# Kernel optimization log

Hardware: AMD Instinct MI355X
Metric: run time of the kernel (lower is better)

The kernel has to match this reference:

```python
import jax, jax.numpy as jnp
import numpy as np
from jax import lax

T, B = 64, 16
N, W, R = 256, 64, 4          # mem_slot, mem_size, read_heads
IN, OUT = 64, 64
NHID, NNOUT = 256, 256
IF_SIZE = W * R + 3 * W + 5 * R + 3  # 471
EPS = 1e-6


def setup_inputs() -> dict:
    key = jax.random.key(0)
    ks = jax.random.split(key, 8)
    in_dim = IN + R * W
    def glorot(k, shape):
        fan_in = shape[0]
        return jax.random.normal(k, shape, dtype=jnp.float32) / np.sqrt(fan_in)
    return {
        "input_data": jax.random.normal(ks[0], (T, B, IN), dtype=jnp.float32),
        "W1": glorot(ks[1], (in_dim, NHID)),
        "b1": jnp.zeros((NHID,), jnp.float32),
        "W2": glorot(ks[2], (NHID, NNOUT)),
        "b2": jnp.zeros((NNOUT,), jnp.float32),
        "W_if": glorot(ks[3], (NNOUT, IF_SIZE)),
        "b_if": jnp.zeros((IF_SIZE,), jnp.float32),
        "W_out": glorot(ks[4], (NNOUT, OUT)),
        "W_mem_out": glorot(ks[5], (R * W, OUT)),
    }


def oneplus(x):
    return 1.0 + jax.nn.softplus(x)


def content_address(mem, keys, strengths):
    # mem [B,N,W], keys [B,W,R], strengths [B,R] -> weights [B,N,R]
    mem_n = mem / (jnp.linalg.norm(mem, axis=-1, keepdims=True) + EPS)
    key_n = keys / (jnp.linalg.norm(keys, axis=1, keepdims=True) + EPS)
    sim = jnp.einsum('bnw,bwr->bnr', mem_n, key_n)
    return jax.nn.softmax(sim * strengths[:, None, :], axis=1)


def parse_interface(z):
    # z: [B, IF_SIZE] -> dict of interface components (NeuCom layout)
    o = 0
    read_keys = z[:, o:o + W * R].reshape(-1, W, R); o += W * R
    read_str = oneplus(z[:, o:o + R]); o += R
    write_key = z[:, o:o + W]; o += W
    write_str = oneplus(z[:, o:o + 1]); o += 1
    erase = jax.nn.sigmoid(z[:, o:o + W]); o += W
    write_vec = z[:, o:o + W]; o += W
    free_gates = jax.nn.sigmoid(z[:, o:o + R]); o += R
    alloc_gate = jax.nn.sigmoid(z[:, o:o + 1]); o += 1
    write_gate = jax.nn.sigmoid(z[:, o:o + 1]); o += 1
    read_modes = jax.nn.softmax(z[:, o:o + 3 * R].reshape(-1, 3, R), axis=1)
    return (read_keys, read_str, write_key, write_str, erase, write_vec,
            free_gates, alloc_gate, write_gate, read_modes)


def _dnc_forward(input_data, W1, b1, W2, b2, W_if, b_if, W_out, W_mem_out):
    Bz = input_data.shape[1]
    eye = jnp.eye(N, dtype=input_data.dtype)

    def step(carry, x_t):
        mem, usage, rw, ww, prec, link, rvec = carry
        # --- controller (feedforward) ---
        ctrl_in = jnp.concatenate([x_t, rvec.reshape(Bz, R * W)], axis=1)
        h = jnp.tanh(ctrl_in @ W1 + b1)
        nn_out = jnp.tanh(h @ W2 + b2)
        (read_keys, read_str, write_key, write_str, erase, write_vec,
         free_gates, alloc_gate, write_gate, read_modes) = parse_interface(nn_out @ W_if + b_if)
        # --- write ---
        retention = jnp.prod(1.0 - free_gates[:, None, :] * rw, axis=2)   # [B,N]
        usage = (usage + ww - usage * ww) * retention
        idx = jnp.argsort(usage, axis=1)                                  # ascending usage
        u_sorted = jnp.take_along_axis(usage, idx, axis=1)
        prod_excl = jnp.concatenate(
            [jnp.ones((Bz, 1), usage.dtype), jnp.cumprod(u_sorted, axis=1)[:, :-1]], axis=1)
        alloc_sorted = (1.0 - u_sorted) * prod_excl
        alloc = jnp.take_along_axis(alloc_sorted, jnp.argsort(idx, axis=1), axis=1)
        wc = content_address(mem, write_key[:, :, None], write_str)[:, :, 0]  # [B,N]
        ww = write_gate * (alloc_gate * alloc + (1.0 - alloc_gate) * wc)
        mem = mem * (1.0 - ww[:, :, None] * erase[:, None, :]) \
              + ww[:, :, None] * write_vec[:, None, :]
        link = (1.0 - ww[:, :, None] - ww[:, None, :]) * link \
               + ww[:, :, None] * prec[:, None, :]
        link = link * (1.0 - eye)
        prec = (1.0 - jnp.sum(ww, axis=1, keepdims=True)) * prec + ww
        # --- read ---
        rc = content_address(mem, read_keys, read_str)                    # [B,N,R]
        fwd_w = jnp.einsum('bnm,bmr->bnr', link, rw)
        bwd_w = jnp.einsum('bmn,bmr->bnr', link, rw)
        rw = (bwd_w * read_modes[:, 0][:, None, :]
              + rc * read_modes[:, 1][:, None, :]
              + fwd_w * read_modes[:, 2][:, None, :])
        rvec = jnp.einsum('bnw,bnr->bwr', mem, rw)                        # [B,W,R]
        out = nn_out @ W_out + rvec.reshape(Bz, R * W) @ W_mem_out
        view = (free_gates, alloc_gate, write_gate, rw, ww, usage)
        return (mem, usage, rw, ww, prec, link, rvec), (out, view)

    carry0 = (
        jnp.full((Bz, N, W), EPS, input_data.dtype),   # mem_mat
        jnp.zeros((Bz, N), input_data.dtype),          # usage
        jnp.zeros((Bz, N, R), input_data.dtype),       # read_weight
        jnp.zeros((Bz, N), input_data.dtype),          # write_weight
        jnp.zeros((Bz, N), input_data.dtype),          # precedence
        jnp.zeros((Bz, N, N), input_data.dtype),       # link matrix
        jnp.zeros((Bz, W, R), input_data.dtype),       # read vectors
    )
    _, (outputs, _view) = lax.scan(step, carry0, input_data)
    return outputs  # [T,B,OUT]


def reference(input_data, W1, b1, W2, b2, W_if, b_if, W_out, W_mem_out):
    return _dnc_forward(input_data, W1, b1, W2, b2, W_if, b_if, W_out, W_mem_out)
```

## Files before the change

kernel.cpp:

```cpp
#include <hip/hip_runtime.h>
#include <hip/hip_fp16.h>
#include <math.h>

#define Tt 64
#define Bb 16
#define Nn 256
#define Ww 64
#define Rr 4
#define INd 64
#define OUTd 64
#define IFS 471
#define EPSf 1e-6f

#define W1OFF   0
#define W2OFF   40960
#define WIFOFF  73728
#define WOUTOFF 134016
#define WMEMOFF 142208
#define WTOT    150400

#define LROW    130
#define LINKB   (256 * LROW * 4)
#define SCRB    16384
#define FIXF    3456
#define SMEM_MAIN (LINKB + SCRB + FIXF * 4)
#define SMEM_FB   (SCRB + FIXF * 4)

#define RWS 132

typedef _Float16 h2v __attribute__((ext_vector_type(2)));
__device__ __forceinline__ float fdot2(__half2 a, __half2 b, float c) {
    return __builtin_amdgcn_fdot2(*(h2v*)&a, *(h2v*)&b, c, false);
}
__device__ __forceinline__ __half2 pkh(float a, float b) {
    auto r = __builtin_amdgcn_cvt_pkrtz(a, b);
    return *(__half2*)&r;
}

__device__ __forceinline__ float rcpf(float x) {
#if __has_builtin(__builtin_amdgcn_rcpf)
    return __builtin_amdgcn_rcpf(x);
#else
    return 1.f / x;
#endif
}
__device__ __forceinline__ float sigm(float x) { return rcpf(1.f + __expf(-x)); }
__device__ __forceinline__ float tanh_fast(float x) {
    float xc = fminf(fmaxf(x, -15.f), 15.f);
    float e = __expf(2.f * xc);
    return (e - 1.f) * rcpf(e + 1.f);
}
__device__ __forceinline__ float oneplus_(float x) {
    return 1.f + fmaxf(x, 0.f) + log1pf(expf(-fabsf(x)));
}
__device__ __forceinline__ float wsum(float v) {
#pragma unroll
    for (int o = 32; o; o >>= 1) v += __shfl_xor(v, o, 64);
    return v;
}
__device__ __forceinline__ float wmaxr(float v) {
#pragma unroll
    for (int o = 32; o; o >>= 1) v = fmaxf(v, __shfl_xor(v, o, 64));
    return v;
}

__device__ __attribute__((noinline)) float gemv_part(
    const __half2* __restrict__ wP, int str, int iters,
    const __half2* __restrict__ vin)
{
    float a[8] = {0.f,0.f,0.f,0.f,0.f,0.f,0.f,0.f};
    float4 h0 = *(const float4*)(wP);
    float4 h1 = *(const float4*)(wP + str);
#pragma unroll 1
    for (int j0 = 0; j0 < iters - 8; j0 += 8) {
        int k8n = (j0 >> 2) + 2;
        float4 n0 = *(const float4*)(wP + (size_t)k8n * str);
        float4 n1 = *(const float4*)(wP + (size_t)(k8n + 1) * str);
        float4 v0 = *(const float4*)(vin + j0);
        float4 v1 = *(const float4*)(vin + j0 + 4);
        const __half2* hh0 = (const __half2*)&h0;
        const __half2* hh1 = (const __half2*)&h1;
        const __half2* vv0 = (const __half2*)&v0;
        const __half2* vv1 = (const __half2*)&v1;
#pragma unroll
        for (int u = 0; u < 4; ++u) a[u]     = fdot2(hh0[u], vv0[u], a[u]);
#pragma unroll
        for (int u = 0; u < 4; ++u) a[4 + u] = fdot2(hh1[u], vv1[u], a[4 + u]);
        h0 = n0; h1 = n1;
    }
    {
        float4 v0 = *(const float4*)(vin + iters - 8);
        float4 v1 = *(const float4*)(vin + iters - 4);
        const __half2* hh0 = (const __half2*)&h0;
        const __half2* hh1 = (const __half2*)&h1;
        const __half2* vv0 = (const __half2*)&v0;
        const __half2* vv1 = (const __half2*)&v1;
#pragma unroll
        for (int u = 0; u < 4; ++u) a[u]     = fdot2(hh0[u], vv0[u], a[u]);
#pragma unroll
        for (int u = 0; u < 4; ++u) a[4 + u] = fdot2(hh1[u], vv1[u], a[4 + u]);
    }
    return ((a[0]+a[1])+(a[2]+a[3])) + ((a[4]+a[5])+(a[6]+a[7]));
}

__global__ void convert_weights(const float* __restrict__ W1, const float* __restrict__ W2,
                                const float* __restrict__ Wif, const float* __restrict__ Wout,
                                const float* __restrict__ Wmem, __half2* __restrict__ wp) {
    int i = blockIdx.x * blockDim.x + threadIdx.x;
    if (i >= WTOT) return;
    float a, b;
    if (i < W2OFF) {
        int q = i & 3, s = i >> 2, n = s & 255, k2 = (s >> 8) * 4 + q;
        a = W1[(2*k2)*256+n];  b = W1[(2*k2+1)*256+n];
    } else if (i < WIFOFF) {
        int t = i - W2OFF;
        int q = t & 3, s = t >> 2, n = s & 255, k2 = (s >> 8) * 4 + q;
        a = W2[(2*k2)*256+n];  b = W2[(2*k2+1)*256+n];
    } else if (i < WOUTOFF) {
        int t = i - WIFOFF;
        int q = t & 3, s = t >> 2, o = s % IFS, k2 = (s / IFS) * 4 + q;
        a = Wif[(2*k2)*IFS+o]; b = Wif[(2*k2+1)*IFS+o];
    } else if (i < WMEMOFF) {
        int t = i - WOUTOFF;
        int q = t & 3, s = t >> 2, n = s & 63, k2 = (s >> 6) * 4 + q;
        a = Wout[(2*k2)*64+n]; b = Wout[(2*k2+1)*64+n];
    } else {
        int t = i - WMEMOFF;
        int q = t & 3, s = t >> 2, n = s & 63, k2 = (s >> 6) * 4 + q;
        a = Wmem[(2*k2)*64+n]; b = Wmem[(2*k2+1)*64+n];
    }
    wp[i] = __floats2half2_rn(a, b);
}

template <bool LLINK>
__global__ __launch_bounds__(1024) void dnc_kernel(
    const float* __restrict__ x, const float* __restrict__ b1,
    const float* __restrict__ b2, const float* __restrict__ bif,
    const __half2* __restrict__ wp,
    __half* __restrict__ memg,
    __half2* __restrict__ memWg,
    __half2* __restrict__ linkg,
    float* __restrict__ out)
{
    extern __shared__ __align__(16) char smem[];
    const int b = blockIdx.x;
    const int tid = threadIdx.x;
    const int lane = tid & 63;
    const int wv = tid >> 6;

    __half2* l2p = (__half2*)smem;
    __half2* gl2 = linkg + (size_t)b * (256 * LROW);
    float* scr   = (float*)(smem + (LLINK ? LINKB : 0));
    __half* scrh = (__half*)scr;
    float* fx    = (float*)((char*)scr + SCRB);

    float*   s_rw    = fx + 0;
    __half2* s_ctrlh = (__half2*)(fx + 1024);
    __half2* s_hh    = (__half2*)(fx + 1184);
    __half2* s_nnh   = (__half2*)(fx + 1312);
    __half2* s_rwh   = (__half2*)(fx + 1440);
    float* s_z     = fx + 1968;
    float* s_usage = fx + 2440;
    float* s_ww    = fx + 2696;
    float* s_prec  = fx + 2952;
    float* s_knorm = fx + 3208;
    float* s_rstr  = fx + 3212;
    float* s_rmode = fx + 3216;
    float* s_sc    = fx + 3228;
    float* s_red   = fx + 3232;
    float* s_er    = fx + 3264;
    __half2* s_keyh = (__half2*)(fx + 3328);
    float* s_srt   = scr + 1024;
    float* s_cp    = scr + 1280;
    __half2* s_keyw2 = (__half2*)(scr + 1280);
    float* s_wcdot = scr + 1536;
    float* s_wcss  = scr + 1792;
    __half2* s_wwh2 = (__half2*)(scr + 2048);
    __half2* s_tmh2 = (__half2*)(scr + 2304);
    unsigned* s_keyu = (unsigned*)(scr + 2560);

    __half*  memh  = memg + (size_t)b * (Ww * Nn);
    __half2* memh2 = (__half2*)memh;
    __half2* memW2 = memWg + (size_t)b * (32 * 256);
    __half*  memWh = (__half*)memW2;

    auto lread = [&](int idx) -> __half2 {
        if constexpr (LLINK) return l2p[idx]; else return gl2[idx];
    };
    auto lwrite = [&](int idx, __half2 v) {
        if constexpr (LLINK) l2p[idx] = v; else gl2[idx] = v;
    };
    auto lread2 = [&](int idx) -> float2 {
        if constexpr (LLINK) return *(const float2*)(l2p + idx);
        else return *(const float2*)(gl2 + idx);
    };

    {
        __half2 z2 = pkh(0.f, 0.f);
#pragma unroll 1
        for (int i = tid; i < 256 * LROW; i += 1024) lwrite(i, z2);
        __half2 e2 = __floats2half2_rn(EPSf, EPSf);
#pragma unroll 1
        for (int j = 0; j < 8; ++j) { memh2[tid + j * 1024] = e2; memW2[tid + j * 1024] = e2; }
        if (tid < 528) s_rwh[tid] = z2;
        if (tid < 32) {
            float2 xv = *(const float2*)&x[b * INd + 2 * tid];
            s_ctrlh[tid] = pkh(xv.x, xv.y);
        } else if (tid < 160) s_ctrlh[tid] = z2;
    }
    if (tid < 256) {
        s_usage[tid] = 0.f; s_ww[tid] = 0.f; s_prec[tid] = 0.f;
        s_rw[tid*4+0] = 0.f; s_rw[tid*4+1] = 0.f; s_rw[tid*4+2] = 0.f; s_rw[tid*4+3] = 0.f;
    }

#pragma unroll 1
    for (int t = 0; t < Tt; ++t) {
        __syncthreads();

        {
            int kc = wv >> 2, o = (wv & 3) * 64 + lane;
            scr[kc * 256 + o] = gemv_part(wp + W1OFF + o * 4 + kc * 10240, 1024, 40,
                                          s_ctrlh + kc * 40);
        }
        __syncthreads();
        if (tid < 256) {
            float v = tanh_fast(b1[tid] + ((scr[tid] + scr[256+tid]) + (scr[512+tid] + scr[768+tid])));
            float pv = __shfl_xor(v, 1, 64);
            if ((tid & 1) == 0) s_hh[tid >> 1] = pkh(v, pv);
        }
        __syncthreads();

        {
            int kc = wv >> 2, o = (wv & 3) * 64 + lane;
            scr[kc * 256 + o] = gemv_part(wp + W2OFF + o * 4 + kc * 8192, 1024, 32,
                                          s_hh + kc * 32);
        }
        __syncthreads();
        if (tid < 256) {
            float v = tanh_fast(b2[tid] + ((scr[tid] + scr[256+tid]) + (scr[512+tid] + scr[768+tid])));
            float pv = __shfl_xor(v, 1, 64);
            if ((tid & 1) == 0) s_nnh[tid >> 1] = pkh(v, pv);
        }
        __syncthreads();

        {
            int kc = wv >> 3, o = (wv & 7) * 64 + lane;
            if (o < IFS)
                scr[kc * 512 + o] = gemv_part(wp + WIFOFF + o * 4 + kc * 30144, 1884, 64,
                                              s_nnh + kc * 64);
        }
        __syncthreads();
        if (tid < IFS) {
            float v = bif[tid] + scr[tid] + scr[512 + tid];
            s_z[tid] = v;
            float pv1 = __shfl_xor(v, 1, 64);
            float pv4 = __shfl_xor(v, 4, 64);
            if (tid < 256) {
                if ((tid & 4) == 0)
                    s_keyh[(tid & 3) * 32 + (tid >> 3)] = pkh(v, pv4);
            } else if (tid >= 260 && tid < 324) {
                if ((tid & 1) == 0)
                    s_keyw2[(tid - 260) >> 1] = pkh(v, pv1);
            } else if (tid >= 453 && tid < 457) {
                s_red[8 + (tid - 453)] = sigm(v);
            }
        }
        __syncthreads();

        if (wv < 4) {
            float vz = s_z[lane * 4 + wv];
            float s = wsum(vz * vz);
            if (lane == 0) s_knorm[wv] = sqrtf(s) + EPSf;
        } else if (wv == 4) {
            float vz = s_z[260 + lane];
            float s = wsum(vz * vz);
            if (lane == 0) s_sc[3] = sqrtf(s) + EPSf;
        } else if (wv == 5) {
            if (lane < 4) s_rstr[lane] = oneplus_(s_z[256 + lane]);
            else if (lane >= 8 && lane < 12) {
                int r = lane - 8;
                float a = s_z[459+r], bm = s_z[463+r], c = s_z[467+r];
                float mx = fmaxf(a, fmaxf(bm, c));
                float ea = __expf(a-mx), eb = __expf(bm-mx), ec = __expf(c-mx);
                float inv = rcpf((ea+eb)+ec);
                s_rmode[0*4+r] = ea*inv; s_rmode[1*4+r] = eb*inv; s_rmode[2*4+r] = ec*inv;
            } else if (lane == 16) s_sc[0] = oneplus_(s_z[324]);
            else if (lane == 17) s_sc[1] = sigm(s_z[457]);
            else if (lane == 18) s_sc[2] = sigm(s_z[458]);
        } else if (wv == 6) {
            s_er[lane] = sigm(s_z[325 + lane]);
        } else if (wv >= 8 && wv < 12) {
            int n = tid - 512;
            float4 rw4 = *(const float4*)&s_rw[n*4];
            float4 fg4 = *(const float4*)&s_red[8];
            float ret = (1.f - fg4.x*rw4.x) * (1.f - fg4.y*rw4.y)
                      * (1.f - fg4.z*rw4.z) * (1.f - fg4.w*rw4.w);
            float u = s_usage[n], wwo = s_ww[n];
            float unew = (u + wwo - u * wwo) * ret;
            s_usage[n] = unew;
            unsigned ub = __float_as_uint(unew);
            s_keyu[2*n]     = (ub << 8) | (unsigned)n;
            s_keyu[2*n + 1] = ub >> 24;
        } else if (wv >= 12) {
            int n = tid - 768;
            const __half2* mW = memW2 + n;
            float dot = 0.f, ssv = 0.f;
#pragma unroll 1
            for (int hf = 0; hf < 2; ++hf) {
                __half2 mv[16], kv[16];
#pragma unroll
                for (int u = 0; u < 16; ++u) mv[u] = mW[(hf * 16 + u) * 256];
                *(float4*)&kv[0]  = *(const float4*)(s_keyw2 + hf*16);
                *(float4*)&kv[4]  = *(const float4*)(s_keyw2 + hf*16 + 4);
                *(float4*)&kv[8]  = *(const float4*)(s_keyw2 + hf*16 + 8);
                *(float4*)&kv[12] = *(const float4*)(s_keyw2 + hf*16 + 12);
#pragma unroll
                for (int u = 0; u < 16; ++u) {
                    ssv = fdot2(mv[u], mv[u], ssv);
                    dot = fdot2(mv[u], kv[u], dot);
                }
            }
            s_wcdot[n] = dot; s_wcss[n] = ssv;
        }
        __syncthreads();

        {
            int q = tid >> 8, n = tid & 255;
            unsigned long long kn = *(const unsigned long long*)&s_keyu[2*n];
            int cnt = 0;
            const unsigned long long* kp = (const unsigned long long*)s_keyu;
            int j0 = q * 64;
#pragma unroll 8
            for (int j = j0; j < j0 + 64; j += 2) {
                ulonglong2 kk = *(const ulonglong2*)&kp[j];
                cnt += (kk.x < kn);
                cnt += (kk.y < kn);
            }
            scr[q * 256 + n] = (float)cnt;
        }
        __syncthreads();

        if (wv == 0) {
            int rk[4]; float uu[4];
#pragma unroll
            for (int i = 0; i < 4; ++i) {
                int n = lane * 4 + i;
                float c = scr[n] + scr[256+n] + scr[512+n] + scr[768+n];
                rk[i] = (int)(c + 0.5f);
                uu[i] = s_usage[n];
                s_srt[rk[i]] = uu[i];
            }
            float4 vs = ((const float4*)s_srt)[lane];
            float p1 = vs.x * vs.y, p2 = p1 * vs.z, tot = p2 * vs.w;
            float incl = tot;
#pragma unroll
            for (int off = 1; off < 64; off <<= 1) {
                float tv = __shfl_up(incl, off, 64);
                if (lane >= off) incl *= tv;
            }
            float excl = __shfl_up(incl, 1, 64);
            if (lane == 0) excl = 1.f;
            float4 o4v; o4v.x = excl; o4v.y = excl*vs.x; o4v.z = excl*p1; o4v.w = excl*p2;
            ((float4*)s_cp)[lane] = o4v;

            float sims[4], mx = -1e30f;
#pragma unroll
            for (int i = 0; i < 4; ++i) {
                int n = lane * 4 + i;
                sims[i] = s_wcdot[n] / ((sqrtf(s_wcss[n]) + EPSf) * s_sc[3]) * s_sc[0];
                mx = fmaxf(mx, sims[i]);
            }
            mx = wmaxr(mx);
            float es[4], ls = 0.f;
#pragma unroll
            for (int i = 0; i < 4; ++i) { es[i] = __expf(sims[i] - mx); ls += es[i]; }
            ls = wsum(ls);
            float ag = s_sc[1], wg = s_sc[2], inv = rcpf(ls), lw = 0.f;
#pragma unroll
            for (int i = 0; i < 4; ++i) {
                int n = lane * 4 + i;
                float alloc = (1.f - uu[i]) * s_cp[rk[i]];
                float wwn = wg * (ag * alloc + (1.f - ag) * es[i] * inv);
                s_ww[n] = wwn; lw += wwn;
                s_wwh2[n] = pkh(wwn, wwn);
                s_tmh2[n] = pkh(1.f - wwn, 1.f - wwn);
            }
            lw = wsum(lw);
            if (lane == 0) s_red[0] = lw;
        }
        __syncthreads();

        if (tid < 512) {
            int kc = tid >> 7, p = tid & 127;
            int c0 = 2 * p, c1 = c0 + 1;
            __half2 wwcp = pkh(s_ww[c0], s_ww[c1]);
            __half2 ptp  = pkh(s_prec[c0], s_prec[c1]);
            float acc[8] = {0,0,0,0,0,0,0,0};
            int kbase = kc * 64;
#pragma unroll 1
            for (int k0 = kbase; k0 < kbase + 64; k0 += 8) {
                __half2 lv[8], tm[8], wk[8];
#pragma unroll
                for (int u = 0; u < 8; ++u) lv[u] = lread((k0 + u) * LROW + p);
                *(float4*)&tm[0] = *(const float4*)(s_tmh2 + k0);
                *(float4*)&tm[4] = *(const float4*)(s_tmh2 + k0 + 4);
                *(float4*)&wk[0] = *(const float4*)(s_wwh2 + k0);
                *(float4*)&wk[4] = *(const float4*)(s_wwh2 + k0 + 4);
                __half2 ln[8];
#pragma unroll
                for (int u = 0; u < 8; ++u)
                    ln[u] = __hfma2(__hsub2(tm[u], wwcp), lv[u], __hmul2(wk[u], ptp));
#pragma unroll
                for (int u = 0; u < 8; ++u)
                    lwrite((k0 + u) * LROW + p, ln[u]);
                int kp0 = k0 >> 1;
                __half2 l0p[4], l1p[4];
#pragma unroll
                for (int i = 0; i < 4; ++i) {
                    unsigned ua = *(unsigned*)&ln[2*i], ub = *(unsigned*)&ln[2*i+1];
                    unsigned r0 = __builtin_amdgcn_perm(ub, ua, 0x05040100u);
                    unsigned r1 = __builtin_amdgcn_perm(ub, ua, 0x07060302u);
                    l0p[i] = *(__half2*)&r0; l1p[i] = *(__half2*)&r1;
                }
#pragma unroll
                for (int r = 0; r < 4; ++r) {
                    __half2 rp[4];
                    *(float4*)rp = *(const float4*)(s_rwh + r * RWS + kp0);
#pragma unroll
                    for (int i = 0; i < 4; ++i) {
                        acc[r]     = fdot2(l0p[i], rp[i], acc[r]);
                        acc[4 + r] = fdot2(l1p[i], rp[i], acc[4 + r]);
                    }
                }
            }
            if ((c0 >> 6) == kc) {
                __half2 d0 = lread(c0 * LROW + p);
                __half2 d1 = lread(c1 * LROW + p);
                float dl0 = __half2float(__low2half(d0));
                float dl1 = __half2float(__high2half(d1));
                unsigned u0 = *(unsigned*)&d0; u0 &= 0xFFFF0000u;
                unsigned u1 = *(unsigned*)&d1; u1 &= 0x0000FFFFu;
                lwrite(c0 * LROW + p, *(__half2*)&u0);
                lwrite(c1 * LROW + p, *(__half2*)&u1);
#pragma unroll
                for (int r = 0; r < 4; ++r) {
                    acc[r]     = fmaf(-dl0, s_rw[c0*4 + r], acc[r]);
                    acc[4 + r] = fmaf(-dl1, s_rw[c1*4 + r], acc[4 + r]);
                }
            }
            __half2* bp = (__half2*)scrh + (kc * 128 + p) * 4;
            bp[0] = pkh(acc[0], acc[1]);
            bp[1] = pkh(acc[2], acc[3]);
            bp[2] = pkh(acc[4], acc[5]);
            bp[3] = pkh(acc[6], acc[7]);
        } else {
            int t0 = tid - 512;
#pragma unroll 1
            for (int jb = 0; jb < 2; ++jb) {
                __half2 mv[8];
#pragma unroll
                for (int j = 0; j < 8; ++j) mv[j] = memh2[t0 + (jb * 8 + j) * 512];
#pragma unroll
                for (int j = 0; j < 8; ++j) {
                    int i2 = t0 + (jb * 8 + j) * 512;
                    int w = i2 >> 7, n2 = i2 & 127;
                    float er = s_er[w];
                    float wvv = s_z[389 + w];
                    float2 mf = __half22float2(mv[j]);
                    float wa = s_ww[2*n2], wb = s_ww[2*n2 + 1];
                    mf.x = mf.x * (1.f - wa * er) + wa * wvv;
                    mf.y = mf.y * (1.f - wb * er) + wb * wvv;
                    __half2 hv = __floats2half2_rn(mf.x, mf.y);
                    memh2[i2] = hv;
                    int wb2 = (w >> 1) * 512 + 4 * n2 + (w & 1);
                    memWh[wb2]     = __low2half(hv);
                    memWh[wb2 + 2] = __high2half(hv);
                }
            }
        }
        __syncthreads();

        {
            int q = tid >> 8, n8 = tid & 255;
            float f[4] = {0.f, 0.f, 0.f, 0.f};
            int base = n8 * LROW + q * 32;
#pragma unroll 1
            for (int j0 = 0; j0 < 32; j0 += 8) {
                __half2 lv[8];
                float2 a0 = lread2(base + j0);
                float2 a1 = lread2(base + j0 + 2);
                float2 a2 = lread2(base + j0 + 4);
                float2 a3 = lread2(base + j0 + 6);
                *(float2*)&lv[0] = a0; *(float2*)&lv[2] = a1;
                *(float2*)&lv[4] = a2; *(float2*)&lv[6] = a3;
#pragma unroll
                for (int r = 0; r < 4; ++r) {
                    __half2 rp[8];
                    *(float4*)&rp[0] = *(const float4*)(s_rwh + r * RWS + q * 32 + j0);
                    *(float4*)&rp[4] = *(const float4*)(s_rwh + r * RWS + q * 32 + j0 + 4);
#pragma unroll
                    for (int u = 0; u < 8; ++u) f[r] = fdot2(lv[u], rp[u], f[r]);
                }
            }
            __half2* fp2 = (__half2*)(scrh + 4096) + (q * 256 + n8) * 2;
            fp2[0] = pkh(f[0], f[1]);
            fp2[1] = pkh(f[2], f[3]);
            if (q == 0) s_prec[n8] = (1.f - s_red[0]) * s_prec[n8] + s_ww[n8];
        }
        __syncthreads();

        int rr = tid >> 8, n8c = tid & 255;
        float bwv = 0.f, fwv = 0.f, e_rc = 0.f;
        {
#pragma unroll
            for (int kc = 0; kc < 4; ++kc)
                bwv += __half2float(scrh[(kc * 128 + (n8c >> 1)) * 8 + (n8c & 1) * 4 + rr]);
#pragma unroll
            for (int qq = 0; qq < 4; ++qq)
                fwv += __half2float(scrh[4096 + (qq * 256 + n8c) * 4 + rr]);
            const __half2* mW = memW2 + n8c;
            const __half2* kh = s_keyh + rr * 32;
            float ssv = 0.f, dv = 0.f;
#pragma unroll 1
            for (int hf = 0; hf < 2; ++hf) {
                __half2 mv[16], kv[16];
#pragma unroll
                for (int u = 0; u < 16; ++u) mv[u] = mW[(hf * 16 + u) * 256];
                *(float4*)&kv[0]  = *(const float4*)(kh + hf*16);
                *(float4*)&kv[4]  = *(const float4*)(kh + hf*16 + 4);
                *(float4*)&kv[8]  = *(const float4*)(kh + hf*16 + 8);
                *(float4*)&kv[12] = *(const float4*)(kh + hf*16 + 12);
#pragma unroll
                for (int u = 0; u < 16; ++u) {
                    ssv = fdot2(mv[u], mv[u], ssv);
                    dv  = fdot2(mv[u], kv[u], dv);
                }
            }
            float sim = dv / ((sqrtf(ssv) + EPSf) * s_knorm[rr]) * s_rstr[rr];
            e_rc = __expf(sim);
            float s = wsum(e_rc);
            if (lane == 0) s_red[16 + wv] = s;
        }
        __syncthreads();
        {
            float sm = (s_red[16+rr*4+0] + s_red[16+rr*4+1]) + (s_red[16+rr*4+2] + s_red[16+rr*4+3]);
            float rc = e_rc * rcpf(sm);
            float v = bwv * s_rmode[0*4+rr] + rc * s_rmode[1*4+rr] + fwv * s_rmode[2*4+rr];
            s_rw[n8c*4 + rr] = v;
            float pv = __shfl_xor(v, 1, 64);
            if ((n8c & 1) == 0) s_rwh[rr * RWS + (n8c >> 1)] = pkh(v, pv);
        }
        __syncthreads();

        {
            int kc = tid >> 8, o = tid & 255, w = o >> 2, r = o & 3;
            const __half2* mw2 = (const __half2*)(memh + w * 256 + kc * 64);
            const __half2* rw2 = s_rwh + r * RWS + kc * 32;
            float a = 0.f;
#pragma unroll
            for (int c = 0; c < 8; ++c) {
                __half2 mv[4], rv[4];
                *(float4*)mv = *(const float4*)(mw2 + c * 4);
                *(float4*)rv = *(const float4*)(rw2 + c * 4);
#pragma unroll
                for (int u = 0; u < 4; ++u) a = fdot2(mv[u], rv[u], a);
            }
            scr[kc * 256 + o] = a;
        }
        __syncthreads();

        if (tid < 256) {
            float v = (scr[tid] + scr[256+tid]) + (scr[512+tid] + scr[768+tid]);
            float pv = __shfl_xor(v, 1, 64);
            if ((tid & 1) == 0) s_ctrlh[32 + (tid >> 1)] = pkh(v, pv);
        } else if (tid >= 512 && tid < 544) {
            if (t + 1 < Tt) {
                int i = tid - 512;
                float2 xv = *(const float2*)&x[((t + 1) * Bb + b) * INd + 2 * i];
                s_ctrlh[i] = pkh(xv.x, xv.y);
            }
        }
        __syncthreads();

        {
            int c4 = wv, o4 = lane;
            const __half2* wsrc = (c4 < 8) ? (wp + WOUTOFF + o4 * 4 + c4 * 1024)
                                           : (wp + WMEMOFF + o4 * 4 + (c4 - 8) * 1024);
            const __half2* vsrc = (c4 < 8) ? (s_nnh + c4 * 16)
                                           : (s_ctrlh + 32 + (c4 - 8) * 16);
            scr[c4 * 64 + o4] = gemv_part(wsrc, 256, 16, vsrc);
        }
        __syncthreads();
        if (tid < 64) {
            float s = 0.f;
#pragma unroll
            for (int g = 0; g < 16; ++g) s += scr[g * 64 + tid];
            out[(t * Bb + b) * OUTd + tid] = s;
        }
    }
}

extern "C" void kernel_launch(void* const* d_in, const int* in_sizes, int n_in,
                              void* d_out, int out_size, void* d_ws, size_t ws_size,
                              hipStream_t stream) {
    const float* x    = (const float*)d_in[0];
    const float* W1   = (const float*)d_in[1];
    const float* b1   = (const float*)d_in[2];
    const float* W2   = (const float*)d_in[3];
    const float* b2   = (const float*)d_in[4];
    const float* Wif  = (const float*)d_in[5];
    const float* bif  = (const float*)d_in[6];
    const float* Wout = (const float*)d_in[7];
    const float* Wmem = (const float*)d_in[8];
    float* out = (float*)d_out;

    char* ws = (char*)d_ws;
    __half2* wp    = (__half2*)ws;
    __half*  memg  = (__half*)(ws + 601600);
    __half2* memWg = (__half2*)(ws + 601600 + 524288);
    __half2* linkg = (__half2*)(ws + 601600 + 524288 + 524288);

    convert_weights<<<dim3((WTOT + 255) / 256), dim3(256), 0, stream>>>(W1, W2, Wif, Wout, Wmem, wp);

    hipError_t rc = hipFuncSetAttribute(
        reinterpret_cast<const void*>(&dnc_kernel<true>),
        hipFuncAttributeMaxDynamicSharedMemorySize, SMEM_MAIN);
    if (rc == hipSuccess) {
        dnc_kernel<true><<<dim3(Bb), dim3(1024), SMEM_MAIN, stream>>>(
            x, b1, b2, bif, wp, memg, memWg, linkg, out);
    } else {
        dnc_kernel<false><<<dim3(Bb), dim3(1024), SMEM_FB, stream>>>(
            x, b1, b2, bif, wp, memg, memWg, linkg, out);
    }
}
```

Baseline: 1.680 ms.

## Replace shared-memory split-K reductions with intra-wave shuffles to drop barriers

After: 1.669 ms. No clear change (-0.6%).

```diff
diff --git a/kernel.cpp b/kernel.cpp
--- a/kernel.cpp
+++ b/kernel.cpp
@@ -212,57 +212,60 @@
         s_usage[tid] = 0.f; s_ww[tid] = 0.f; s_prec[tid] = 0.f;
         s_rw[tid*4+0] = 0.f; s_rw[tid*4+1] = 0.f; s_rw[tid*4+2] = 0.f; s_rw[tid*4+3] = 0.f;
     }
+    __syncthreads();
 
 #pragma unroll 1
     for (int t = 0; t < Tt; ++t) {
-        __syncthreads();
-
-        {
-            int kc = wv >> 2, o = (wv & 3) * 64 + lane;
-            scr[kc * 256 + o] = gemv_part(wp + W1OFF + o * 4 + kc * 10240, 1024, 40,
-                                          s_ctrlh + kc * 40);
-        }
-        __syncthreads();
-        if (tid < 256) {
-            float v = tanh_fast(b1[tid] + ((scr[tid] + scr[256+tid]) + (scr[512+tid] + scr[768+tid])));
-            float pv = __shfl_xor(v, 1, 64);
-            if ((tid & 1) == 0) s_hh[tid >> 1] = pkh(v, pv);
-        }
-        __syncthreads();
-
-        {
-            int kc = wv >> 2, o = (wv & 3) * 64 + lane;
-            scr[kc * 256 + o] = gemv_part(wp + W2OFF + o * 4 + kc * 8192, 1024, 32,
-                                          s_hh + kc * 32);
-        }
-        __syncthreads();
-        if (tid < 256) {
-            float v = tanh_fast(b2[tid] + ((scr[tid] + scr[256+tid]) + (scr[512+tid] + scr[768+tid])));
-            float pv = __shfl_xor(v, 1, 64);
-            if ((tid & 1) == 0) s_nnh[tid >> 1] = pkh(v, pv);
-        }
-        __syncthreads();
-
-        {
-            int kc = wv >> 3, o = (wv & 7) * 64 + lane;
+        {
+            int o = (wv << 4) + (lane & 15), kc = lane >> 4;
+            float a = gemv_part(wp + W1OFF + o * 4 + kc * 10240, 1024, 40,
+                                s_ctrlh + kc * 40);
+            a += __shfl_xor(a, 16, 64);
+            a += __shfl_xor(a, 32, 64);
+            if (lane < 16) {
+                float v = tanh_fast(b1[o] + a);
+                float pv = __shfl_xor(v, 1, 64);
+                if ((lane & 1) == 0) s_hh[o >> 1] = pkh(v, pv);
+            }
+        }
+        __syncthreads();
+
+        {
+            int o = (wv << 4) + (lane & 15), kc = lane >> 4;
+            float a = gemv_part(wp + W2OFF + o * 4 + kc * 8192, 1024, 32,
+                                s_hh + kc * 32);
+            a += __shfl_xor(a, 16, 64);
+            a += __shfl_xor(a, 32, 64);
+            if (lane < 16) {
+                float v = tanh_fast(b2[o] + a);
+                float pv = __shfl_xor(v, 1, 64);
+                if ((lane & 1) == 0) s_nnh[o >> 1] = pkh(v, pv);
+            }
+        }
+        __syncthreads();
+
+        {
+            int o = (wv << 5) + (lane & 31);
+            int kc = lane >> 5;
+            float a = 0.f;
             if (o < IFS)
-                scr[kc * 512 + o] = gemv_part(wp + WIFOFF + o * 4 + kc * 30144, 1884, 64,
-                                              s_nnh + kc * 64);
-        }
-        __syncthreads();
-        if (tid < IFS) {
-            float v = bif[tid] + scr[tid] + scr[512 + tid];
-            s_z[tid] = v;
-            float pv1 = __shfl_xor(v, 1, 64);
-            float pv4 = __shfl_xor(v, 4, 64);
-            if (tid < 256) {
-                if ((tid & 4) == 0)
-                    s_keyh[(tid & 3) * 32 + (tid >> 3)] = pkh(v, pv4);
-            } else if (tid >= 260 && tid < 324) {
-                if ((tid & 1) == 0)
-                    s_keyw2[(tid - 260) >> 1] = pkh(v, pv1);
-            } else if (tid >= 453 && tid < 457) {
-                s_red[8 + (tid - 453)] = sigm(v);
+                a = gemv_part(wp + WIFOFF + o * 4 + kc * 30144, 1884, 64,
+                              s_nnh + kc * 64);
+            a += __shfl_xor(a, 32, 64);
+            if (lane < 32 && o < IFS) {
+                float v = bif[o] + a;
+                s_z[o] = v;
+                float pv1 = __shfl_xor(v, 1, 64);
+                float pv4 = __shfl_xor(v, 4, 64);
+                if (o < 256) {
+                    if ((o & 4) == 0)
+                        s_keyh[(o & 3) * 32 + (o >> 3)] = pkh(v, pv4);
+                } else if (o >= 260 && o < 324) {
+                    if ((o & 1) == 0)
+                        s_keyw2[(o - 260) >> 1] = pkh(v, pv1);
+                } else if (o >= 453 && o < 457) {
+                    s_red[8 + (o - 453)] = sigm(v);
+                }
             }
         }
         __syncthreads();
@@ -553,7 +556,8 @@
         __syncthreads();
 
         {
-            int kc = tid >> 8, o = tid & 255, w = o >> 2, r = o & 3;
+            int o = (wv << 4) + (lane & 15), kc = lane >> 4;
+            int w = o >> 2, r = o & 3;
             const __half2* mw2 = (const __half2*)(memh + w * 256 + kc * 64);
             const __half2* rw2 = s_rwh + r * RWS + kc * 32;
             float a = 0.f;
@@ -565,17 +569,14 @@
 #pragma unroll
                 for (int u = 0; u < 4; ++u) a = fdot2(mv[u], rv[u], a);
             }
-            scr[kc * 256 + o] = a;
-        }
-        __syncthreads();
-
-        if (tid < 256) {
-            float v = (scr[tid] + scr[256+tid]) + (scr[512+tid] + scr[768+tid]);
-            float pv = __shfl_xor(v, 1, 64);
-            if ((tid & 1) == 0) s_ctrlh[32 + (tid >> 1)] = pkh(v, pv);
-        } else if (tid >= 512 && tid < 544) {
-            if (t + 1 < Tt) {
-                int i = tid - 512;
+            a += __shfl_xor(a, 16, 64);
+            a += __shfl_xor(a, 32, 64);
+            if (lane < 16) {
+                float pv = __shfl_xor(a, 1, 64);
+                if ((lane & 1) == 0) s_ctrlh[32 + (o >> 1)] = pkh(a, pv);
+            }
+            if (wv < 2 && lane >= 48 && t + 1 < Tt) {
+                int i = (wv << 4) + (lane - 48);
                 float2 xv = *(const float2*)&x[((t + 1) * Bb + b) * INd + 2 * i];
                 s_ctrlh[i] = pkh(xv.x, xv.y);
             }
@@ -583,19 +584,17 @@
         __syncthreads();
 
         {
-            int c4 = wv, o4 = lane;
-            const __half2* wsrc = (c4 < 8) ? (wp + WOUTOFF + o4 * 4 + c4 * 1024)
-                                           : (wp + WMEMOFF + o4 * 4 + (c4 - 8) * 1024);
-            const __half2* vsrc = (c4 < 8) ? (s_nnh + c4 * 16)
-                                           : (s_ctrlh + 32 + (c4 - 8) * 16);
-            scr[c4 * 64 + o4] = gemv_part(wsrc, 256, 16, vsrc);
-        }
-        __syncthreads();
-        if (tid < 64) {
-            float s = 0.f;
-#pragma unroll
-            for (int g = 0; g < 16; ++g) s += scr[g * 64 + tid];
-            out[(t * Bb + b) * OUTd + tid] = s;
+            int o = (wv << 2) + (lane & 3), c = lane >> 2;
+            const __half2* wsrc = (c < 8) ? (wp + WOUTOFF + o * 4 + c * 1024)
+                                          : (wp + WMEMOFF + o * 4 + (c - 8) * 1024);
+            const __half2* vsrc = (c < 8) ? (s_nnh + c * 16)
+                                          : (s_ctrlh + 32 + (c - 8) * 16);
+            float a = gemv_part(wsrc, 256, 16, vsrc);
+            a += __shfl_xor(a, 4, 64);
+            a += __shfl_xor(a, 8, 64);
+            a += __shfl_xor(a, 16, 64);
+            a += __shfl_xor(a, 32, 64);
+            if (lane < 4) out[(t * Bb + b) * OUTd + o] = a;
         }
     }
 }
```
